# Optimization experiments

Measured on AMD Instinct MI355X. Metric: run time of the kernel, lower is better.

## Reference

```python
import jax, jax.numpy as jnp
import numpy as np

N = 50000
E = 800000
F_IN = 128
HID = 16
HEADS = 8
CLS = 16
NEG_SLOPE = 0.2


def setup_inputs() -> dict:
    key = jax.random.key(0)
    ks = jax.random.split(key, 12)
    x = jax.random.normal(ks[0], (N, F_IN), dtype=jnp.float32)
    edge_index = jax.random.randint(ks[1], (2, E), 0, N, dtype=jnp.int32)
    s = 0.1
    W1 = jax.random.normal(ks[2], (F_IN, HEADS * HID), dtype=jnp.float32) * s
    att_src1 = jax.random.normal(ks[3], (HEADS, HID), dtype=jnp.float32) * s
    att_dst1 = jax.random.normal(ks[4], (HEADS, HID), dtype=jnp.float32) * s
    b1 = jax.random.normal(ks[5], (HEADS * HID,), dtype=jnp.float32) * s
    W2 = jax.random.normal(ks[6], (HEADS * HID, CLS), dtype=jnp.float32) * s
    att_src2 = jax.random.normal(ks[7], (1, CLS), dtype=jnp.float32) * s
    att_dst2 = jax.random.normal(ks[8], (1, CLS), dtype=jnp.float32) * s
    b2 = jax.random.normal(ks[9], (CLS,), dtype=jnp.float32) * s
    return {"x": x, "edge_index": edge_index, "W1": W1, "att_src1": att_src1,
            "att_dst1": att_dst1, "b1": b1, "W2": W2, "att_src2": att_src2,
            "att_dst2": att_dst2, "b2": b2}


def _gat_conv(x, src, dst, W, a_src, a_dst, b, heads, out_ch, concat):
    n = x.shape[0]
    h = (x @ W).reshape(n, heads, out_ch)                     # [N,H,C]
    alpha_src = (h * a_src[None]).sum(-1)                     # [N,H]
    alpha_dst = (h * a_dst[None]).sum(-1)                     # [N,H]
    e = jax.nn.leaky_relu(alpha_src[src] + alpha_dst[dst], NEG_SLOPE)  # [E,H]
    m = jax.lax.stop_gradient(jax.ops.segment_max(e, dst, num_segments=n))
    e = jnp.exp(e - m[dst])
    denom = jax.ops.segment_sum(e, dst, num_segments=n)
    alpha = e / (denom[dst] + 1e-16)                          # [E,H]
    msg = h[src] * alpha[:, :, None]                          # [E,H,C]
    out = jax.ops.segment_sum(msg, dst, num_segments=n)       # [N,H,C]
    out = out.reshape(n, heads * out_ch) if concat else out.mean(axis=1)
    return out + b


def reference(x, edge_index, W1, att_src1, att_dst1, b1, W2, att_src2, att_dst2, b2):
    # PyG GATConv default add_self_loops=True
    loop = jnp.arange(N, dtype=edge_index.dtype)
    src = jnp.concatenate([edge_index[0], loop])
    dst = jnp.concatenate([edge_index[1], loop])
    h = _gat_conv(x, src, dst, W1, att_src1, att_dst1, b1, HEADS, HID, True)
    h = jax.nn.elu(h)
    # dropout inactive (eval mode)
    out = _gat_conv(h, src, dst, W2, att_src2, att_dst2, b2, 1, CLS, False)
    return out
```

## Files before the change

### kernel.cpp

```cpp
#include <hip/hip_runtime.h>
#include <hip/hip_bf16.h>
#include <limits.h>
#include <math.h>

#define N 50000
#define E_ 800000
#define ETOT 850000
#define HH 128
#define HEADS 8
#define HID 16
#define CLS 16
#define NEG 0.2f
#define NB ((N + 255) / 256)
#define GEMM_NB ((N + 63) / 64)
#define LINK_NB ((ETOT + 255) / 256)

typedef unsigned short u16;
typedef unsigned int   u32;
typedef unsigned long long u64;

__device__ __forceinline__ u16 f2bu(float f){
  union{float f; u32 i;} c; c.f = f;
  u32 lsb = (c.i >> 16) & 1u;
  c.i += 0x7fffu + lsb;
  return (u16)(c.i >> 16);
}
__device__ __forceinline__ float blo(u32 u){ union{u32 i; float f;} c; c.i = u << 16; return c.f; }
__device__ __forceinline__ float bhi(u32 u){ union{u32 i; float f;} c; c.i = u & 0xffff0000u; return c.f; }

#define BM 64
#define BKK 32
__global__ __launch_bounds__(256) void k_gemm1link(const float* __restrict__ x,
                                                   const float* __restrict__ W,
                                                   const float* __restrict__ Asv,
                                                   const float* __restrict__ Adv,
                                                   u16* __restrict__ h1b,
                                                   float* __restrict__ as1,
                                                   float* __restrict__ ad1,
                                                   const int* __restrict__ ei,
                                                   int* __restrict__ deg,
                                                   int* __restrict__ head,
                                                   u64* __restrict__ next_src){
  __shared__ float xT[BKK*BM];
  __shared__ float Wl[BKK*128];
  if(blockIdx.x >= GEMM_NB){
    int e = (blockIdx.x - GEMM_NB)*256 + threadIdx.x;
    if(e < ETOT){
      int s, d;
      if(e < E_){ s = ei[e]; d = ei[E_ + e]; } else { s = d = e - E_; }
      atomicAdd(&deg[d], 1);
      int old = atomicExch(&head[d], e);
      next_src[e] = ((u64)(u32)s << 32) | (u32)old;
    }
    return;
  }
  int tid = threadIdx.x;
  int row0 = blockIdx.x * BM;
  int tx = tid & 15;
  int ty = tid >> 4;
  float acc[4][8];
  #pragma unroll
  for(int r=0;r<4;r++)
    #pragma unroll
    for(int j=0;j<8;j++) acc[r][j]=0.f;

  int lr = tid >> 2;
  int lk = (tid & 3) * 8;
  int wr = tid >> 3;
  int wc = (tid & 7) * 16;
  int xrow = row0 + lr; if(xrow >= N) xrow = N-1;
  const float* xbase = x + (size_t)xrow*128;

  for(int k0=0; k0<128; k0+=BKK){
    float4 v0 = *(const float4*)(xbase + k0 + lk);
    float4 v1 = *(const float4*)(xbase + k0 + lk + 4);
    float4 wv0, wv1, wv2, wv3;
    {
      const float4* wsrc = (const float4*)(W + (size_t)(k0+wr)*128 + wc);
      wv0 = wsrc[0]; wv1 = wsrc[1]; wv2 = wsrc[2]; wv3 = wsrc[3];
    }
    __syncthreads();
    xT[(lk+0)*BM + lr] = v0.x;
    xT[(lk+1)*BM + lr] = v0.y;
    xT[(lk+2)*BM + lr] = v0.z;
    xT[(lk+3)*BM + lr] = v0.w;
    xT[(lk+4)*BM + lr] = v1.x;
    xT[(lk+5)*BM + lr] = v1.y;
    xT[(lk+6)*BM + lr] = v1.z;
    xT[(lk+7)*BM + lr] = v1.w;
    {
      char* wl = (char*)Wl;
      int swz = (wr & 7) << 4;
      int b = (wr*128 + wc)*4;
      *(float4*)(wl + ((b      ) ^ swz)) = wv0;
      *(float4*)(wl + ((b + 16 ) ^ swz)) = wv1;
      *(float4*)(wl + ((b + 32 ) ^ swz)) = wv2;
      *(float4*)(wl + ((b + 48 ) ^ swz)) = wv3;
    }
    __syncthreads();
    #pragma unroll 8
    for(int k=0;k<BKK;k++){
      float4 xv = *(const float4*)&xT[k*BM + ty*4];
      const char* wl = (const char*)Wl;
      int swz = (k & 7) << 4;
      float4 wa = *(const float4*)(wl + ((k*512 + tx*16      ) ^ swz));
      float4 wb = *(const float4*)(wl + ((k*512 + 256 + tx*16) ^ swz));
      float xr[4] = {xv.x, xv.y, xv.z, xv.w};
      #pragma unroll
      for(int r=0;r<4;r++){
        acc[r][0] = fmaf(xr[r], wa.x, acc[r][0]);
        acc[r][1] = fmaf(xr[r], wa.y, acc[r][1]);
        acc[r][2] = fmaf(xr[r], wa.z, acc[r][2]);
        acc[r][3] = fmaf(xr[r], wa.w, acc[r][3]);
        acc[r][4] = fmaf(xr[r], wb.x, acc[r][4]);
        acc[r][5] = fmaf(xr[r], wb.y, acc[r][5]);
        acc[r][6] = fmaf(xr[r], wb.z, acc[r][6]);
        acc[r][7] = fmaf(xr[r], wb.w, acc[r][7]);
      }
    }
  }
  float as_lo[4], as_hi[4], ad_lo[4], ad_hi[4];
  #pragma unroll
  for(int j=0;j<4;j++){
    as_lo[j] = Asv[tx*4+j];      ad_lo[j] = Adv[tx*4+j];
    as_hi[j] = Asv[64+tx*4+j];   ad_hi[j] = Adv[64+tx*4+j];
  }
  int q = tx >> 2;
  #pragma unroll
  for(int r=0;r<4;r++){
    int row = row0 + ty*4 + r;
    float ps_lo=0.f, ps_hi=0.f, pd_lo=0.f, pd_hi=0.f;
    #pragma unroll
    for(int j=0;j<4;j++){
      ps_lo = fmaf(acc[r][j],   as_lo[j], ps_lo);
      pd_lo = fmaf(acc[r][j],   ad_lo[j], pd_lo);
      ps_hi = fmaf(acc[r][4+j], as_hi[j], ps_hi);
      pd_hi = fmaf(acc[r][4+j], ad_hi[j], pd_hi);
    }
    ps_lo += __shfl_xor(ps_lo,1); ps_lo += __shfl_xor(ps_lo,2);
    pd_lo += __shfl_xor(pd_lo,1); pd_lo += __shfl_xor(pd_lo,2);
    ps_hi += __shfl_xor(ps_hi,1); ps_hi += __shfl_xor(ps_hi,2);
    pd_hi += __shfl_xor(pd_hi,1); pd_hi += __shfl_xor(pd_hi,2);
    if(row < N){
      u16* dst = h1b + (size_t)row*128;
      ushort4 a, b;
      a.x=f2bu(acc[r][0]); a.y=f2bu(acc[r][1]); a.z=f2bu(acc[r][2]); a.w=f2bu(acc[r][3]);
      b.x=f2bu(acc[r][4]); b.y=f2bu(acc[r][5]); b.z=f2bu(acc[r][6]); b.w=f2bu(acc[r][7]);
      *(ushort4*)(dst + tx*4)      = a;
      *(ushort4*)(dst + 64 + tx*4) = b;
      if((tx & 3) == 0){
        as1[row*8 + q]     = ps_lo;  as1[row*8 + 4 + q] = ps_hi;
        ad1[row*8 + q]     = pd_lo;  ad1[row*8 + 4 + q] = pd_hi;
      }
    }
  }
}

__global__ __launch_bounds__(256) void k_scan1(const int* __restrict__ deg, int* __restrict__ bsum){
  __shared__ int sm[256];
  int t = threadIdx.x;
  int i = blockIdx.x*256 + t;
  sm[t] = (i < N) ? deg[i] : 0;
  __syncthreads();
  #pragma unroll
  for(int ofs=128; ofs>0; ofs>>=1){
    if(t < ofs) sm[t] += sm[t+ofs];
    __syncthreads();
  }
  if(t == 0) bsum[blockIdx.x] = sm[0];
}

__global__ __launch_bounds__(256) void k_scan2(const int* __restrict__ bsum,
                                               int* __restrict__ boff,
                                               int* __restrict__ off){
  __shared__ int sm[256];
  int t = threadIdx.x;
  sm[t] = (t < NB) ? bsum[t] : 0;
  __syncthreads();
  #pragma unroll
  for(int ofs=1; ofs<256; ofs<<=1){
    int v = sm[t];
    int add = (t >= ofs) ? sm[t-ofs] : 0;
    __syncthreads();
    sm[t] = v + add;
    __syncthreads();
  }
  if(t < NB) boff[t] = (t == 0) ? 0 : sm[t-1];
  if(t == 255) off[N] = sm[NB-1];
}

__global__ __launch_bounds__(256) void k_scan3walk(const int* __restrict__ deg,
                                                   const int* __restrict__ boff,
                                                   const int* __restrict__ head,
                                                   const u64* __restrict__ next_src,
                                                   int* __restrict__ off,
                                                   int* __restrict__ csr){
  __shared__ int sm[256];
  int t = threadIdx.x;
  int i = blockIdx.x*256 + t;
  int v0 = (i < N) ? deg[i] : 0;
  sm[t] = v0;
  __syncthreads();
  #pragma unroll
  for(int ofs=1; ofs<256; ofs<<=1){
    int v = sm[t];
    int add = (t >= ofs) ? sm[t-ofs] : 0;
    __syncthreads();
    sm[t] = v + add;
    __syncthreads();
  }
  if(i < N){
    int excl = boff[blockIdx.x] + sm[t] - v0;
    off[i] = excl;
    int e = head[i];
    int pos = excl;
    while(e >= 0){
      u64 v = next_src[e];
      csr[pos++] = (int)(v >> 32);
      e = (int)(u32)(v & 0xffffffffu);
    }
  }
}

#define CH 32
__global__ __launch_bounds__(256) void k_agg1(const int* __restrict__ off,
                                              const int* __restrict__ csr,
                                              const float* __restrict__ as1,
                                              const float* __restrict__ ad1,
                                              const u32* __restrict__ h1w,
                                              const float* __restrict__ b1,
                                              u32* __restrict__ helu_w){
  __shared__ float wsm[4][CH*8];
  __shared__ int   ssm[4][CH];
  int wv   = threadIdx.x >> 6;
  int lane = threadIdx.x & 63;
  int node = blockIdx.x*4 + wv;
  int beg = off[node], end = off[node+1];
  int h  = lane >> 3;
  int hh = lane & 7;
  int el = lane >> 3;
  float advA = ad1[node*8 + hh];
  float den = 0.f, num0 = 0.f, num1 = 0.f;
  float* wsw = wsm[wv];
  int*   ssw = ssm[wv];
  for(int base = beg; base < end; base += CH){
    int cnt = end - base; if(cnt > CH) cnt = CH;
    #pragma unroll
    for(int k=0;k<CH;k+=8){
      int e = el + k;
      if(e < cnt){
        int s = csr[base+e];
        if(hh == 0) ssw[e] = s;
        float v = as1[s*8+hh] + advA;
        v = v > 0.f ? v : NEG*v;
        wsw[e*8+hh] = __expf(v);
      }
    }
    int e = 0;
    for(; e+4 <= cnt; e += 4){
      int s0 = ssw[e], s1 = ssw[e+1], s2 = ssw[e+2], s3 = ssw[e+3];
      float w0 = wsw[e*8+h], w1 = wsw[e*8+8+h], w2 = wsw[e*8+16+h], w3 = wsw[e*8+24+h];
      u32 u0 = h1w[(size_t)s0*64 + lane];
      u32 u1 = h1w[(size_t)s1*64 + lane];
      u32 u2 = h1w[(size_t)s2*64 + lane];
      u32 u3 = h1w[(size_t)s3*64 + lane];
      den += (w0+w1)+(w2+w3);
      num0 = fmaf(w0, blo(u0), num0); num1 = fmaf(w0, bhi(u0), num1);
      num0 = fmaf(w1, blo(u1), num0); num1 = fmaf(w1, bhi(u1), num1);
      num0 = fmaf(w2, blo(u2), num0); num1 = fmaf(w2, bhi(u2), num1);
      num0 = fmaf(w3, blo(u3), num0); num1 = fmaf(w3, bhi(u3), num1);
    }
    for(; e < cnt; e++){
      int s = ssw[e];
      float w = wsw[e*8+h];
      u32 u = h1w[(size_t)s*64 + lane];
      den += w;
      num0 = fmaf(w, blo(u), num0);
      num1 = fmaf(w, bhi(u), num1);
    }
  }
  float2 bb = ((const float2*)b1)[lane];
  float inv = 1.f / (den + 1e-16f);
  float r0 = num0*inv + bb.x;
  float r1 = num1*inv + bb.y;
  r0 = r0 > 0.f ? r0 : expm1f(r0);
  r1 = r1 > 0.f ? r1 : expm1f(r1);
  helu_w[(size_t)node*64 + lane] = (u32)f2bu(r0) | ((u32)f2bu(r1) << 16);
}

__global__ __launch_bounds__(256) void k_gemm2(const u16* __restrict__ hb,
                                               const float* __restrict__ W2,
                                               const float* __restrict__ Asv,
                                               const float* __restrict__ Adv,
                                               u16* __restrict__ h2b,
                                               float* __restrict__ as2,
                                               float* __restrict__ ad2){
  __shared__ float Wl[128*16];
  int tid = threadIdx.x;
  const float4* W4 = (const float4*)W2;
  float4* Wl4 = (float4*)Wl;
  Wl4[tid]       = W4[tid];
  Wl4[tid + 256] = W4[tid + 256];
  __syncthreads();
  int i = blockIdx.x*16 + (tid >> 4);
  int c = tid & 15;
  if(i >= N) return;
  const uint4* h8 = (const uint4*)(hb + (size_t)i*HH);
  float acc = 0.f;
  #pragma unroll
  for(int ch=0; ch<16; ch++){
    uint4 u = h8[ch];
    int k = ch*8;
    acc = fmaf(blo(u.x), Wl[(k+0)*16+c], acc);
    acc = fmaf(bhi(u.x), Wl[(k+1)*16+c], acc);
    acc = fmaf(blo(u.y), Wl[(k+2)*16+c], acc);
    acc = fmaf(bhi(u.y), Wl[(k+3)*16+c], acc);
    acc = fmaf(blo(u.z), Wl[(k+4)*16+c], acc);
    acc = fmaf(bhi(u.z), Wl[(k+5)*16+c], acc);
    acc = fmaf(blo(u.w), Wl[(k+6)*16+c], acc);
    acc = fmaf(bhi(u.w), Wl[(k+7)*16+c], acc);
  }
  h2b[(size_t)i*CLS + c] = f2bu(acc);
  float ps = acc * Asv[c];
  float pd = acc * Adv[c];
  ps += __shfl_xor(ps,1); ps += __shfl_xor(ps,2); ps += __shfl_xor(ps,4); ps += __shfl_xor(ps,8);
  pd += __shfl_xor(pd,1); pd += __shfl_xor(pd,2); pd += __shfl_xor(pd,4); pd += __shfl_xor(pd,8);
  if(c == 0){ as2[i] = ps; ad2[i] = pd; }
}

__global__ __launch_bounds__(256) void k_agg2(const int* __restrict__ off,
                                              const int* __restrict__ csr,
                                              const float* __restrict__ as2,
                                              const float* __restrict__ ad2,
                                              const u32* __restrict__ h2w,
                                              const float* __restrict__ b2,
                                              float* __restrict__ outp){
  int t = threadIdx.x;
  int node = blockIdx.x*32 + (t >> 3);
  int c2 = t & 7;
  if(node >= N) return;
  int beg = off[node], end = off[node+1];
  float adv = ad2[node];
  float den = 0.f, num0 = 0.f, num1 = 0.f;
  for(int base = beg; base < end; base += 8){
    int cnt = end - base; if(cnt > 8) cnt = 8;
    float w_my = 0.f; int s_my = 0;
    if(c2 < cnt){
      s_my = csr[base + c2];
      float v = as2[s_my] + adv;
      v = v > 0.f ? v : NEG*v;
      w_my = __expf(v);
    }
    #pragma unroll
    for(int j=0; j<8; j++){
      if(j >= cnt) break;
      int src = (t & 56) | j;
      float w = __shfl(w_my, src);
      int   s = __shfl(s_my, src);
      u32 u = h2w[(size_t)s*8 + c2];
      den += w;
      num0 = fmaf(w, blo(u), num0);
      num1 = fmaf(w, bhi(u), num1);
    }
  }
  float inv = 1.f / (den + 1e-16f);
  float2 bb = ((const float2*)b2)[c2];
  float2 r;
  r.x = num0*inv + bb.x;
  r.y = num1*inv + bb.y;
  ((float2*)outp)[(size_t)node*8 + c2] = r;
}

extern "C" void kernel_launch(void* const* d_in, const int* in_sizes, int n_in,
                              void* d_out, int out_size, void* d_ws, size_t ws_size,
                              hipStream_t stream){
  const float* x     = (const float*)d_in[0];
  const int*   ei    = (const int*)  d_in[1];
  const float* W1    = (const float*)d_in[2];
  const float* av_s1 = (const float*)d_in[3];
  const float* av_d1 = (const float*)d_in[4];
  const float* b1    = (const float*)d_in[5];
  const float* W2    = (const float*)d_in[6];
  const float* av_s2 = (const float*)d_in[7];
  const float* av_d2 = (const float*)d_in[8];
  const float* b2    = (const float*)d_in[9];
  float* outp = (float*)d_out;

  char* p = (char*)d_ws;
  auto alloc = [&](size_t bytes){ char* q = p; p += (bytes + 255) & ~(size_t)255; return q; };
  u16*   h1b    = (u16*)  alloc((size_t)N*HH*2);
  u16*   helu_b = (u16*)  alloc((size_t)N*HH*2);
  u16*   h2b    = (u16*)  alloc((size_t)N*CLS*2);
  float* as1    = (float*)alloc((size_t)N*HEADS*4);
  float* ad1    = (float*)alloc((size_t)N*HEADS*4);
  float* as2    = (float*)alloc((size_t)N*4);
  float* ad2    = (float*)alloc((size_t)N*4);
  int*   deg    = (int*)  alloc((size_t)N*4);
  int*   head   = (int*)  alloc((size_t)N*4);
  int*   off    = (int*)  alloc((size_t)(N+1)*4);
  int*   csr    = (int*)  alloc((size_t)ETOT*4);
  u64*   nsrc   = (u64*)  alloc((size_t)ETOT*8);
  int*   bsum   = (int*)  alloc((size_t)NB*4);
  int*   boff   = (int*)  alloc((size_t)NB*4);

  hipMemsetAsync(deg, 0, (size_t)N*4, stream);
  hipMemsetAsync(head, 0xFF, (size_t)N*4, stream);

  k_gemm1link<<<GEMM_NB + LINK_NB, 256, 0, stream>>>(x, W1, av_s1, av_d1, h1b, as1, ad1,
                                                     ei, deg, head, nsrc);
  k_scan1<<<NB, 256, 0, stream>>>(deg, bsum);
  k_scan2<<<1, 256, 0, stream>>>(bsum, boff, off);
  k_scan3walk<<<NB, 256, 0, stream>>>(deg, boff, head, nsrc, off, csr);

  k_agg1<<<N/4, 256, 0, stream>>>(off, csr, as1, ad1, (const u32*)h1b, b1, (u32*)helu_b);

  k_gemm2<<<(N+15)/16, 256, 0, stream>>>(helu_b, W2, av_s2, av_d2, h2b, as2, ad2);
  k_agg2<<<(N+31)/32, 256, 0, stream>>>(off, csr, as2, ad2, (const u32*)h2b, b2, outp);
}
```

Measured before the change: 172.4 us.

## Move layer-1 GEMM to split-bf16 MFMA and restructure edge linking

Replaces the scalar FP32 layer-1 GEMM with a bf16 MFMA kernel. It splits x and W into high and low bf16 parts and uses three products to keep near-FP32 accuracy, with W pre-transposed by a small prep kernel. The attention logits are now computed in a separate kernel from the bf16 h1, which adds an extra pass and computes them from rounded values. Edge linking moves to its own kernel without degree atomics, and degrees are counted by walking the linked lists in the scan. This adds more launches and a second list traversal.

```diff
diff --git a/kernel.cpp b/kernel.cpp
--- a/kernel.cpp
+++ b/kernel.cpp
@@ -12,12 +12,12 @@
 #define CLS 16
 #define NEG 0.2f
 #define NB ((N + 255) / 256)
-#define GEMM_NB ((N + 63) / 64)
-#define LINK_NB ((ETOT + 255) / 256)
 
 typedef unsigned short u16;
 typedef unsigned int   u32;
 typedef unsigned long long u64;
+typedef short s8v __attribute__((ext_vector_type(8)));
+typedef float f4v __attribute__((ext_vector_type(4)));
 
 __device__ __forceinline__ u16 f2bu(float f){
   union{float f; u32 i;} c; c.f = f;
@@ -25,142 +25,161 @@
   c.i += 0x7fffu + lsb;
   return (u16)(c.i >> 16);
 }
+__device__ __forceinline__ float bu2f(u16 u){
+  union{u32 i; float f;} c; c.i = ((u32)u) << 16; return c.f;
+}
 __device__ __forceinline__ float blo(u32 u){ union{u32 i; float f;} c; c.i = u << 16; return c.f; }
 __device__ __forceinline__ float bhi(u32 u){ union{u32 i; float f;} c; c.i = u & 0xffff0000u; return c.f; }
 
-#define BM 64
-#define BKK 32
-__global__ __launch_bounds__(256) void k_gemm1link(const float* __restrict__ x,
-                                                   const float* __restrict__ W,
-                                                   const float* __restrict__ Asv,
-                                                   const float* __restrict__ Adv,
-                                                   u16* __restrict__ h1b,
-                                                   float* __restrict__ as1,
-                                                   float* __restrict__ ad1,
-                                                   const int* __restrict__ ei,
+__global__ __launch_bounds__(256) void k_prepW(const float* __restrict__ W,
+                                               u16* __restrict__ wth, u16* __restrict__ wtl){
+  int i = blockIdx.x*256 + threadIdx.x;
+  if(i >= 128*128) return;
+  int k = i >> 7, c = i & 127;
+  float v = W[i];
+  u16 hi = f2bu(v);
+  u16 lo = f2bu(v - bu2f(hi));
+  wth[c*128 + k] = hi;
+  wtl[c*128 + k] = lo;
+}
+
+__global__ __launch_bounds__(256) void k_link(const int* __restrict__ ei,
+                                              int* __restrict__ head,
+                                              int* __restrict__ srcv,
+                                              int* __restrict__ nxt){
+  int e = blockIdx.x*256 + threadIdx.x;
+  if(e >= ETOT) return;
+  int s, d;
+  if(e < E_){ s = ei[e]; d = ei[E_ + e]; } else { s = d = e - E_; }
+  int old = atomicExch(&head[d], e);
+  srcv[e] = s;
+  nxt[e]  = old;
+}
+
+#define GBM 64
+__global__ __launch_bounds__(256) void k_gemm1m(const float* __restrict__ x,
+                                                const u16* __restrict__ wth,
+                                                const u16* __restrict__ wtl,
+                                                u16* __restrict__ h1b){
+  __shared__ u16 xh[GBM][40], xl[GBM][40];
+  __shared__ u16 wh[128][40], wl[128][40];
+  int tid  = threadIdx.x;
+  int wv   = tid >> 6;
+  int lane = tid & 63;
+  int row0 = blockIdx.x * GBM;
+
+  f4v acc[4][2];
+  #pragma unroll
+  for(int t=0;t<4;t++)
+    #pragma unroll
+    for(int u=0;u<2;u++) acc[t][u] = (f4v){0.f,0.f,0.f,0.f};
+
+  int xr  = tid >> 2;
+  int xkq = (tid & 3) * 8;
+  int wc  = tid & 127;
+  int wq  = (tid >> 7) * 8;
+  int xrow = row0 + xr; if(xrow >= N) xrow = N-1;
+  const float* xb = x + (size_t)xrow*128 + xkq;
+  int fr = lane & 15, fg = lane >> 4;
+  int kk = fg*8;
+
+  for(int kc=0; kc<4; kc++){
+    int k0 = kc*32;
+    float4 v0 = *(const float4*)(xb + k0);
+    float4 v1 = *(const float4*)(xb + k0 + 4);
+    __syncthreads();
+    {
+      float vv[8] = {v0.x,v0.y,v0.z,v0.w,v1.x,v1.y,v1.z,v1.w};
+      s8v H, L;
+      #pragma unroll
+      for(int j=0;j<8;j++){
+        u16 h_ = f2bu(vv[j]);
+        H[j] = (short)h_;
+        L[j] = (short)f2bu(vv[j] - bu2f(h_));
+      }
+      *(s8v*)&xh[xr][xkq] = H;
+      *(s8v*)&xl[xr][xkq] = L;
+    }
+    #pragma unroll
+    for(int j=0;j<2;j++){
+      int kq = wq + j*16;
+      *(s8v*)&wh[wc][kq] = *(const s8v*)&wth[wc*128 + k0 + kq];
+      *(s8v*)&wl[wc][kq] = *(const s8v*)&wtl[wc*128 + k0 + kq];
+    }
+    __syncthreads();
+    s8v a_h[4], a_l[4], b_h[2], b_l[2];
+    #pragma unroll
+    for(int t=0;t<4;t++){
+      a_h[t] = *(const s8v*)&xh[t*16 + fr][kk];
+      a_l[t] = *(const s8v*)&xl[t*16 + fr][kk];
+    }
+    #pragma unroll
+    for(int u=0;u<2;u++){
+      int col = wv*32 + u*16 + fr;
+      b_h[u] = *(const s8v*)&wh[col][kk];
+      b_l[u] = *(const s8v*)&wl[col][kk];
+    }
+    #pragma unroll
+    for(int t=0;t<4;t++){
+      #pragma unroll
+      for(int u=0;u<2;u++){
+        acc[t][u] = __builtin_amdgcn_mfma_f32_16x16x32_bf16(a_h[t], b_h[u], acc[t][u], 0,0,0);
+        acc[t][u] = __builtin_amdgcn_mfma_f32_16x16x32_bf16(a_h[t], b_l[u], acc[t][u], 0,0,0);
+        acc[t][u] = __builtin_amdgcn_mfma_f32_16x16x32_bf16(a_l[t], b_h[u], acc[t][u], 0,0,0);
+      }
+    }
+  }
+  #pragma unroll
+  for(int t=0;t<4;t++){
+    #pragma unroll
+    for(int j=0;j<4;j++){
+      int row = row0 + t*16 + fg*4 + j;
+      if(row < N){
+        u16* dst = h1b + (size_t)row*128 + wv*32 + fr;
+        dst[0]  = f2bu(acc[t][0][j]);
+        dst[16] = f2bu(acc[t][1][j]);
+      }
+    }
+  }
+}
+
+__global__ __launch_bounds__(256) void k_alpha1(const u16* __restrict__ h1b,
+                                                const float* __restrict__ Asv,
+                                                const float* __restrict__ Adv,
+                                                float* __restrict__ as1,
+                                                float* __restrict__ ad1){
+  int id = blockIdx.x*256 + threadIdx.x;
+  if(id >= N*HEADS) return;
+  int i = id >> 3, h = id & 7;
+  const uint4* hv = (const uint4*)(h1b + (size_t)i*HH + h*HID);
+  uint4 u0 = hv[0], u1 = hv[1];
+  float vals[16] = {blo(u0.x),bhi(u0.x),blo(u0.y),bhi(u0.y),
+                    blo(u0.z),bhi(u0.z),blo(u0.w),bhi(u0.w),
+                    blo(u1.x),bhi(u1.x),blo(u1.y),bhi(u1.y),
+                    blo(u1.z),bhi(u1.z),blo(u1.w),bhi(u1.w)};
+  float s=0.f, d=0.f;
+  #pragma unroll
+  for(int j=0;j<16;j++){
+    s = fmaf(vals[j], Asv[h*HID+j], s);
+    d = fmaf(vals[j], Adv[h*HID+j], d);
+  }
+  as1[id]=s; ad1[id]=d;
+}
+
+__global__ __launch_bounds__(256) void k_scan1walk(const int* __restrict__ head,
+                                                   const int* __restrict__ nxt,
                                                    int* __restrict__ deg,
-                                                   int* __restrict__ head,
-                                                   u64* __restrict__ next_src){
-  __shared__ float xT[BKK*BM];
-  __shared__ float Wl[BKK*128];
-  if(blockIdx.x >= GEMM_NB){
-    int e = (blockIdx.x - GEMM_NB)*256 + threadIdx.x;
-    if(e < ETOT){
-      int s, d;
-      if(e < E_){ s = ei[e]; d = ei[E_ + e]; } else { s = d = e - E_; }
-      atomicAdd(&deg[d], 1);
-      int old = atomicExch(&head[d], e);
-      next_src[e] = ((u64)(u32)s << 32) | (u32)old;
-    }
-    return;
-  }
-  int tid = threadIdx.x;
-  int row0 = blockIdx.x * BM;
-  int tx = tid & 15;
-  int ty = tid >> 4;
-  float acc[4][8];
-  #pragma unroll
-  for(int r=0;r<4;r++)
-    #pragma unroll
-    for(int j=0;j<8;j++) acc[r][j]=0.f;
-
-  int lr = tid >> 2;
-  int lk = (tid & 3) * 8;
-  int wr = tid >> 3;
-  int wc = (tid & 7) * 16;
-  int xrow = row0 + lr; if(xrow >= N) xrow = N-1;
-  const float* xbase = x + (size_t)xrow*128;
-
-  for(int k0=0; k0<128; k0+=BKK){
-    float4 v0 = *(const float4*)(xbase + k0 + lk);
-    float4 v1 = *(const float4*)(xbase + k0 + lk + 4);
-    float4 wv0, wv1, wv2, wv3;
-    {
-      const float4* wsrc = (const float4*)(W + (size_t)(k0+wr)*128 + wc);
-      wv0 = wsrc[0]; wv1 = wsrc[1]; wv2 = wsrc[2]; wv3 = wsrc[3];
-    }
-    __syncthreads();
-    xT[(lk+0)*BM + lr] = v0.x;
-    xT[(lk+1)*BM + lr] = v0.y;
-    xT[(lk+2)*BM + lr] = v0.z;
-    xT[(lk+3)*BM + lr] = v0.w;
-    xT[(lk+4)*BM + lr] = v1.x;
-    xT[(lk+5)*BM + lr] = v1.y;
-    xT[(lk+6)*BM + lr] = v1.z;
-    xT[(lk+7)*BM + lr] = v1.w;
-    {
-      char* wl = (char*)Wl;
-      int swz = (wr & 7) << 4;
-      int b = (wr*128 + wc)*4;
-      *(float4*)(wl + ((b      ) ^ swz)) = wv0;
-      *(float4*)(wl + ((b + 16 ) ^ swz)) = wv1;
-      *(float4*)(wl + ((b + 32 ) ^ swz)) = wv2;
-      *(float4*)(wl + ((b + 48 ) ^ swz)) = wv3;
-    }
-    __syncthreads();
-    #pragma unroll 8
-    for(int k=0;k<BKK;k++){
-      float4 xv = *(const float4*)&xT[k*BM + ty*4];
-      const char* wl = (const char*)Wl;
-      int swz = (k & 7) << 4;
-      float4 wa = *(const float4*)(wl + ((k*512 + tx*16      ) ^ swz));
-      float4 wb = *(const float4*)(wl + ((k*512 + 256 + tx*16) ^ swz));
-      float xr[4] = {xv.x, xv.y, xv.z, xv.w};
-      #pragma unroll
-      for(int r=0;r<4;r++){
-        acc[r][0] = fmaf(xr[r], wa.x, acc[r][0]);
-        acc[r][1] = fmaf(xr[r], wa.y, acc[r][1]);
-        acc[r][2] = fmaf(xr[r], wa.z, acc[r][2]);
-        acc[r][3] = fmaf(xr[r], wa.w, acc[r][3]);
-        acc[r][4] = fmaf(xr[r], wb.x, acc[r][4]);
-        acc[r][5] = fmaf(xr[r], wb.y, acc[r][5]);
-        acc[r][6] = fmaf(xr[r], wb.z, acc[r][6]);
-        acc[r][7] = fmaf(xr[r], wb.w, acc[r][7]);
-      }
-    }
-  }
-  float as_lo[4], as_hi[4], ad_lo[4], ad_hi[4];
-  #pragma unroll
-  for(int j=0;j<4;j++){
-    as_lo[j] = Asv[tx*4+j];      ad_lo[j] = Adv[tx*4+j];
-    as_hi[j] = Asv[64+tx*4+j];   ad_hi[j] = Adv[64+tx*4+j];
-  }
-  int q = tx >> 2;
-  #pragma unroll
-  for(int r=0;r<4;r++){
-    int row = row0 + ty*4 + r;
-    float ps_lo=0.f, ps_hi=0.f, pd_lo=0.f, pd_hi=0.f;
-    #pragma unroll
-    for(int j=0;j<4;j++){
-      ps_lo = fmaf(acc[r][j],   as_lo[j], ps_lo);
-      pd_lo = fmaf(acc[r][j],   ad_lo[j], pd_lo);
-      ps_hi = fmaf(acc[r][4+j], as_hi[j], ps_hi);
-      pd_hi = fmaf(acc[r][4+j], ad_hi[j], pd_hi);
-    }
-    ps_lo += __shfl_xor(ps_lo,1); ps_lo += __shfl_xor(ps_lo,2);
-    pd_lo += __shfl_xor(pd_lo,1); pd_lo += __shfl_xor(pd_lo,2);
-    ps_hi += __shfl_xor(ps_hi,1); ps_hi += __shfl_xor(ps_hi,2);
-    pd_hi += __shfl_xor(pd_hi,1); pd_hi += __shfl_xor(pd_hi,2);
-    if(row < N){
-      u16* dst = h1b + (size_t)row*128;
-      ushort4 a, b;
-      a.x=f2bu(acc[r][0]); a.y=f2bu(acc[r][1]); a.z=f2bu(acc[r][2]); a.w=f2bu(acc[r][3]);
-      b.x=f2bu(acc[r][4]); b.y=f2bu(acc[r][5]); b.z=f2bu(acc[r][6]); b.w=f2bu(acc[r][7]);
-      *(ushort4*)(dst + tx*4)      = a;
-      *(ushort4*)(dst + 64 + tx*4) = b;
-      if((tx & 3) == 0){
-        as1[row*8 + q]     = ps_lo;  as1[row*8 + 4 + q] = ps_hi;
-        ad1[row*8 + q]     = pd_lo;  ad1[row*8 + 4 + q] = pd_hi;
-      }
-    }
-  }
-}
-
-__global__ __launch_bounds__(256) void k_scan1(const int* __restrict__ deg, int* __restrict__ bsum){
+                                                   int* __restrict__ bsum){
   __shared__ int sm[256];
   int t = threadIdx.x;
   int i = blockIdx.x*256 + t;
-  sm[t] = (i < N) ? deg[i] : 0;
+  int cnt = 0;
+  if(i < N){
+    int e = head[i];
+    while(e >= 0){ cnt++; e = nxt[e]; }
+    deg[i] = cnt;
+  }
+  sm[t] = cnt;
   __syncthreads();
   #pragma unroll
   for(int ofs=128; ofs>0; ofs>>=1){
@@ -192,7 +211,8 @@
 __global__ __launch_bounds__(256) void k_scan3walk(const int* __restrict__ deg,
                                                    const int* __restrict__ boff,
                                                    const int* __restrict__ head,
-                                                   const u64* __restrict__ next_src,
+                                                   const int* __restrict__ srcv,
+                                                   const int* __restrict__ nxt,
                                                    int* __restrict__ off,
                                                    int* __restrict__ csr){
   __shared__ int sm[256];
@@ -215,9 +235,8 @@
     int e = head[i];
     int pos = excl;
     while(e >= 0){
-      u64 v = next_src[e];
-      csr[pos++] = (int)(v >> 32);
-      e = (int)(u32)(v & 0xffffffffu);
+      csr[pos++] = srcv[e];
+      e = nxt[e];
     }
   }
 }
@@ -399,18 +418,24 @@
   int*   head   = (int*)  alloc((size_t)N*4);
   int*   off    = (int*)  alloc((size_t)(N+1)*4);
   int*   csr    = (int*)  alloc((size_t)ETOT*4);
-  u64*   nsrc   = (u64*)  alloc((size_t)ETOT*8);
+  int*   srcv   = (int*)  alloc((size_t)ETOT*4);
+  int*   nxt    = (int*)  alloc((size_t)ETOT*4);
+  u16*   wth    = (u16*)  alloc((size_t)128*128*2);
+  u16*   wtl    = (u16*)  alloc((size_t)128*128*2);
   int*   bsum   = (int*)  alloc((size_t)NB*4);
   int*   boff   = (int*)  alloc((size_t)NB*4);
 
-  hipMemsetAsync(deg, 0, (size_t)N*4, stream);
   hipMemsetAsync(head, 0xFF, (size_t)N*4, stream);
 
-  k_gemm1link<<<GEMM_NB + LINK_NB, 256, 0, stream>>>(x, W1, av_s1, av_d1, h1b, as1, ad1,
-                                                     ei, deg, head, nsrc);
-  k_scan1<<<NB, 256, 0, stream>>>(deg, bsum);
+  k_link<<<(ETOT+255)/256, 256, 0, stream>>>(ei, head, srcv, nxt);
+  k_prepW<<<(128*128+255)/256, 256, 0, stream>>>(W1, wth, wtl);
+
+  k_gemm1m<<<(N+GBM-1)/GBM, 256, 0, stream>>>(x, wth, wtl, h1b);
+  k_alpha1<<<(N*HEADS+255)/256, 256, 0, stream>>>(h1b, av_s1, av_d1, as1, ad1);
+
+  k_scan1walk<<<NB, 256, 0, stream>>>(head, nxt, deg, bsum);
   k_scan2<<<1, 256, 0, stream>>>(bsum, boff, off);
-  k_scan3walk<<<NB, 256, 0, stream>>>(deg, boff, head, nsrc, off, csr);
+  k_scan3walk<<<NB, 256, 0, stream>>>(deg, boff, head, srcv, nxt, off, csr);
 
   k_agg1<<<N/4, 256, 0, stream>>>(off, csr, as1, ad1, (const u32*)h1b, b1, (u32*)helu_b);
 
```

Result: no change. 171.1 us (-0.8%).
